# Kernel tuning notes

Measured on AMD Instinct MI355X. Metric: run time of the kernel, lower is better.

The kernel has to match this reference:

```python
import jax, jax.numpy as jnp
import numpy as np
from jax import lax

T, B, F, H = 128, 256, 512, 1024
NEG_SLOPE = 0.01  # torch LeakyReLU default


def leaky_relu(x):
    return jnp.where(x >= 0, x, NEG_SLOPE * x)


def setup_inputs() -> dict:
    key = jax.random.key(0)
    ks = jax.random.split(key, 10)
    s1 = 1.0 / np.sqrt(F)
    sh = 1.0 / np.sqrt(H)
    return {
        "x": jax.random.normal(ks[0], (T, B, F), dtype=jnp.float32),
        "dones": jax.random.randint(ks[1], (T, B), 0, 2, dtype=jnp.int32),
        "W1": jax.random.uniform(ks[2], (H, F), jnp.float32, -s1, s1),
        "b1": jax.random.uniform(ks[3], (H,), jnp.float32, -s1, s1),
        "W_ih": jax.random.uniform(ks[4], (4 * H, H), jnp.float32, -sh, sh),
        "W_hh": jax.random.uniform(ks[5], (4 * H, H), jnp.float32, -sh, sh),
        "b_ih": jax.random.uniform(ks[6], (4 * H,), jnp.float32, -sh, sh),
        "b_hh": jax.random.uniform(ks[7], (4 * H,), jnp.float32, -sh, sh),
        "Wv": jax.random.uniform(ks[8], (1, H), jnp.float32, -sh, sh),
        "bv": jax.random.uniform(ks[9], (1,), jnp.float32, -sh, sh),
    }


def _forward(x, dones, W1, b1, W_ih, W_hh, b_ih, b_hh, Wv, bv):
    # shared_net: Linear + LeakyReLU, applied to all timesteps at once
    shared = leaky_relu(jnp.einsum("tbf,hf->tbh", x, W1) + b1)  # [T,B,H]
    # precompute input contribution to all gates (i,f,g,o order as in torch)
    x_gates = jnp.einsum("tbh,gh->tbg", shared, W_ih) + b_ih + b_hh  # [T,B,4H]
    reset = (dones == 0).astype(x.dtype)[:, :, None]  # [T,B,1], 0 where done

    def step(carry, inp):
        h, c = carry  # [B,H] each
        xg, m = inp
        # mask-reset hidden state where episode ended, then detach (torch .detach())
        h = lax.stop_gradient(h * m)
        c = lax.stop_gradient(c * m)
        gates = xg + h @ W_hh.T  # [B,4H]
        i, f, g, o = jnp.split(gates, 4, axis=-1)
        i = jax.nn.sigmoid(i)
        f = jax.nn.sigmoid(f)
        g = jnp.tanh(g)
        o = jax.nn.sigmoid(o)
        c = f * c + i * g
        h = o * jnp.tanh(c)
        return (h, c), h

    h0 = jnp.zeros((x.shape[1], W_hh.shape[1]), x.dtype)
    (hT, cT), hs = lax.scan(step, (h0, h0), (x_gates, reset))
    value = leaky_relu(hs) @ Wv.T + bv  # [T,B,1]
    hidden = jnp.stack([hT, cT], axis=0)  # [2*num_layers, B, H]
    return value, hidden


def reference(x, dones, W1, b1, W_ih, W_hh, b_ih, b_hh, Wv, bv):
    return _forward(x, dones, W1, b1, W_ih, W_hh, b_ih, b_hh, Wv, bv)
```

## Files before the change

### kernel.cpp

```cpp
#include <hip/hip_runtime.h>
#include <cstdint>
#include <cstddef>

#define T_DIM 128
#define B_DIM 256
#define F_DIM 512
#define H_DIM 1024
#define G_DIM 4096

typedef unsigned short u16;
typedef unsigned short u16x8 __attribute__((ext_vector_type(8)));
typedef unsigned short u16x4 __attribute__((ext_vector_type(4)));
typedef __bf16 bf16x8 __attribute__((ext_vector_type(8)));
typedef float f32x4 __attribute__((ext_vector_type(4)));
typedef unsigned long long u64;

__device__ __forceinline__ float bf2f(u16 u) {
    union { unsigned v; float f; } x; x.v = ((unsigned)u) << 16; return x.f;
}
__device__ __forceinline__ u16 f2bf(float f) {
    union { float f; unsigned v; } x; x.f = f;
    return (u16)((x.v + 0x7fffu + ((x.v >> 16) & 1u)) >> 16);
}

__device__ __forceinline__ f32x4 mfma16(u16x8 a, u16x8 b, f32x4 c) {
    return __builtin_amdgcn_mfma_f32_16x16x32_bf16(
        __builtin_bit_cast(bf16x8, a), __builtin_bit_cast(bf16x8, b), c, 0, 0, 0);
}

template <int AUX>
__device__ __forceinline__ void gl_lds16(const void* g, void* s) {
    __builtin_amdgcn_global_load_lds(
        (const __attribute__((address_space(1))) void*)g,
        (__attribute__((address_space(3))) void*)s, 16, 0, AUX);
}

__device__ __forceinline__ float sigm(float x) { return 1.0f / (1.0f + __expf(-x)); }
__device__ __forceinline__ float tanh_fast(float x) {
    float e = __expf(2.0f * x);
    return 1.0f - 2.0f / (e + 1.0f);
}

template <int EPI>
__global__ __launch_bounds__(256) void gemm_bt128(
    const u16* __restrict__ A, const u16* __restrict__ B,
    const float* __restrict__ bias, u16* __restrict__ C, int K, int N) {
    __shared__ __align__(16) u16 smem[128 * 136];
    u16* lA = smem;
    u16* lB = smem + 8192;
    const int lane = threadIdx.x & 63;
    const int wave = threadIdx.x >> 6;
    const int wr = wave >> 1, wc = wave & 1;
    const int bm = blockIdx.x, bn = blockIdx.y;
    f32x4 acc[4][4] = {};
    const int srow = lane >> 3;
    const int scol = (lane & 7) * 8;
    const u16* Abase = A + (size_t)(bm * 128 + srow) * K + scol;
    const u16* Bbase = B + (size_t)(bn * 128 + srow) * K + scol;

    for (int k0 = 0; k0 < K; k0 += 64) {
#pragma unroll
        for (int j = 0; j < 4; ++j) {
            int chunk = wave * 4 + j;
            gl_lds16<0>(Abase + (size_t)(chunk * 8) * K + k0, lA + chunk * 512);
            gl_lds16<0>(Bbase + (size_t)(chunk * 8) * K + k0, lB + chunk * 512);
        }
        __syncthreads();
        const u16* pA = lA + (wr * 64 + (lane & 15)) * 64 + (lane >> 4) * 8;
        const u16* pB = lB + (wc * 64 + (lane & 15)) * 64 + (lane >> 4) * 8;
#pragma unroll
        for (int kk = 0; kk < 2; ++kk) {
            u16x8 a[4], b[4];
#pragma unroll
            for (int m = 0; m < 4; ++m) a[m] = *(const u16x8*)(pA + m * 1024 + kk * 32);
#pragma unroll
            for (int n = 0; n < 4; ++n) b[n] = *(const u16x8*)(pB + n * 1024 + kk * 32);
#pragma unroll
            for (int m = 0; m < 4; ++m)
#pragma unroll
                for (int n = 0; n < 4; ++n)
                    acc[m][n] = mfma16(a[m], b[n], acc[m][n]);
        }
        __syncthreads();
    }
#pragma unroll
    for (int n = 0; n < 4; ++n) {
        int cc = wc * 64 + n * 16 + (lane & 15);
        float bv = bias[bn * 128 + cc];
#pragma unroll
        for (int m = 0; m < 4; ++m) {
            int rr = wr * 64 + m * 16 + ((lane >> 4) * 4);
#pragma unroll
            for (int i = 0; i < 4; ++i) {
                float v = acc[m][n][i] + bv;
                if (EPI == 1) v = (v >= 0.0f) ? v : 0.01f * v;
                smem[(rr + i) * 136 + cc] = f2bf(v);
            }
        }
    }
    __syncthreads();
#pragma unroll
    for (int p = 0; p < 8; ++p) {
        int rr = p * 16 + wave * 4 + (lane >> 4);
        int cc = (lane & 15) * 8;
        u16x8 v = *(const u16x8*)(smem + rr * 136 + cc);
        *(u16x8*)(C + (size_t)(bm * 128 + rr) * N + bn * 128 + cc) = v;
    }
}


__device__ __forceinline__ void stage_chunk_blk(const char* hinB, int bm, char* buf,
                                                int kc, int wave, int lane) {
#pragma unroll
    for (int j = 0; j < 8; ++j) {
        int hr = wave * 8 + j;
        int r = hr * 2 + (lane >> 5);
        int sc = ((lane & 31) * 16) ^ ((r & 7) << 4);
        int cbg = kc * 512 + sc;
        gl_lds16<17>(hinB + (size_t)(cbg >> 5) * 8192 + bm * 2048 + r * 32 + (cbg & 31),
                     buf + (size_t)hr * 1024);
    }
}

__global__ __launch_bounds__(256, 1) void lstm_seq(
    const u16* __restrict__ xg, const u16* __restrict__ Whh,
    const int* __restrict__ dones, const float* __restrict__ Wv,
    u16* __restrict__ h0, u16* __restrict__ h1,
    float* __restrict__ cbuf, float* __restrict__ hbuf,
    float* __restrict__ value, int* __restrict__ flags,
    float* __restrict__ vpartial, int t0, int nt, int first) {
    __shared__ __align__(16) char sm[65536];
    float* lepi = (float*)sm;
    char* hbB = sm + 17408;
    float* vpB = (float*)(sm + 19456);
    const int tid = threadIdx.x;
    const int lane = tid & 63, wave = tid >> 6;
    const int bm = blockIdx.x & 3, bn = blockIdx.x >> 2;
    const int sw = (lane & 7) << 4;

    u16x8 breg[32];
    {
        const u16* wrow = Whh + (size_t)(bn * 64 + wave * 16 + (lane & 15)) * H_DIM +
                          (lane >> 4) * 8;
#pragma unroll
        for (int s = 0; s < 32; ++s) breg[s] = *(const u16x8*)(wrow + s * 32);
    }

    const int r = tid & 63;
    const int ublk = tid >> 6;
    const int bg = bm * 64 + r;
    const int ucol = bn * 16 + ublk * 4;
    float wv[4], c[4];
#pragma unroll
    for (int uu = 0; uu < 4; ++uu) wv[uu] = Wv[ucol + uu];
    if (first) {
        c[0] = c[1] = c[2] = c[3] = 0.0f;
    } else {
        float4 cv = *(const float4*)(cbuf + (size_t)bg * H_DIM + ucol);
        c[0] = cv.x; c[1] = cv.y; c[2] = cv.z; c[3] = cv.w;
    }

    const int rl = lane & 15;
    const int ko = (lane >> 4) * 16;

    for (int tt = 0; tt < nt; ++tt) {
        const int t = t0 + tt;
        const char* hinB = (const char*)((t & 1) ? h1 : h0);
        u16* houtB = (t & 1) ? h0 : h1;

        auto poll16 = [&](int kc) {
            if (t > 0) {
                const int fi = bm * 64 + kc * 16 + (lane & 15);
                while (__hip_atomic_load(&flags[fi], __ATOMIC_RELAXED,
                                         __HIP_MEMORY_SCOPE_AGENT) < t)
                    __builtin_amdgcn_s_sleep(1);
            }
        };

        const int done = dones[t * B_DIM + bg];
        u16x4 xv[4];
#pragma unroll
        for (int uu = 0; uu < 4; ++uu)
            xv[uu] = *(const u16x4*)(xg + (size_t)tt * B_DIM * G_DIM +
                                     (size_t)bg * G_DIM + bn * 64 + (ublk * 4 + uu) * 4);

        poll16(0);
        stage_chunk_blk(hinB, bm, sm, 0, wave, lane);
        poll16(1);
        __syncthreads();

        f32x4 acc[4] = {};
#pragma unroll
        for (int kc = 0; kc < 4; ++kc) {
            char* buf = sm + (kc & 1) * 32768;
            if (kc < 3) stage_chunk_blk(hinB, bm, sm + ((kc + 1) & 1) * 32768, kc + 1,
                                        wave, lane);
#pragma unroll
            for (int s2 = 0; s2 < 8; ++s2) {
                int kb2 = s2 * 64 + ko;
#pragma unroll
                for (int m = 0; m < 4; ++m) {
                    u16x8 a = *(const u16x8*)(buf + (m * 16 + rl) * 512 + (kb2 ^ sw));
                    acc[m] = mfma16(a, breg[kc * 8 + s2], acc[m]);
                }
            }
            if (kc < 2) poll16(kc + 2);
            if (kc < 3) __syncthreads();
        }

        if (t > 0 && tid < 64) {
            const float* vp = vpartial + (size_t)((t - 1) & 1) * 65536 +
                              (size_t)lane * 1024 + (size_t)(bm * 64 + bn) * 4;
            union { u64 u; float f[2]; } ua, ub;
            ua.u = __hip_atomic_load((const u64*)vp, __ATOMIC_RELAXED,
                                     __HIP_MEMORY_SCOPE_AGENT);
            ub.u = __hip_atomic_load((const u64*)(vp + 2), __ATOMIC_RELAXED,
                                     __HIP_MEMORY_SCOPE_AGENT);
            float s = ua.f[0] + ua.f[1] + ub.f[0] + ub.f[1];
#pragma unroll
            for (int m2 = 32; m2 >= 1; m2 >>= 1) s += __shfl_xor(s, m2);
            if (tid == 0) value[(t - 1) * B_DIM + bm * 64 + bn] += s;
        }

#pragma unroll
        for (int m = 0; m < 4; ++m)
#pragma unroll
            for (int i = 0; i < 4; ++i)
                lepi[(m * 16 + (lane >> 4) * 4 + i) * 65 + wave * 16 + rl] = acc[m][i];

        const float mb = (done == 0) ? 1.0f : 0.0f;
        float vpart = 0.0f;
        u16x4 hb;
        float hf[4];
#pragma unroll
        for (int uu = 0; uu < 4; ++uu) {
            const float* gp = &lepi[r * 65 + (ublk * 4 + uu) * 4];
            float gi = bf2f(xv[uu][0]) + mb * gp[0];
            float gf = bf2f(xv[uu][1]) + mb * gp[1];
            float gg = bf2f(xv[uu][2]) + mb * gp[2];
            float go = bf2f(xv[uu][3]) + mb * gp[3];
            float i_ = sigm(gi), f_ = sigm(gf), g_ = tanh_fast(gg), o_ = sigm(go);
            float cn = f_ * (mb * c[uu]) + i_ * g_;
            float hn = o_ * tanh_fast(cn);
            c[uu] = cn; hf[uu] = hn;
            hb[uu] = f2bf(hn);
            float lr = (hn >= 0.0f) ? hn : 0.01f * hn;
            vpart += lr * wv[uu];
        }
        *(u16x4*)(hbB + r * 32 + ublk * 8) = hb;
        vpB[r * 4 + ublk] = vpart;
        if (t == T_DIM - 1)
            *(float4*)(hbuf + (size_t)bg * H_DIM + ucol) = make_float4(hf[0], hf[1], hf[2], hf[3]);
        __syncthreads();

        {
            u64 hv = *(const u64*)(hbB + tid * 8);
            __hip_atomic_store((u64*)((char*)houtB + (size_t)bn * 8192 + bm * 2048 + tid * 8),
                               hv, __ATOMIC_RELAXED, __HIP_MEMORY_SCOPE_AGENT);
            if (tid < 64) {
                const u64* pv = (const u64*)vpB + tid * 2;
                u64 v0 = pv[0], v1 = pv[1];
                float* dv = vpartial + (size_t)(t & 1) * 65536 + (size_t)bn * 1024 +
                            bm * 256 + tid * 4;
                __hip_atomic_store((u64*)dv, v0, __ATOMIC_RELAXED, __HIP_MEMORY_SCOPE_AGENT);
                __hip_atomic_store((u64*)dv + 1, v1, __ATOMIC_RELAXED, __HIP_MEMORY_SCOPE_AGENT);
            }
        }
        __syncthreads();
        if (tid == 0)
            __hip_atomic_store(&flags[bm * 64 + bn], t + 1, __ATOMIC_RELAXED,
                               __HIP_MEMORY_SCOPE_AGENT);
    }
    *(float4*)(cbuf + (size_t)bg * H_DIM + ucol) = make_float4(c[0], c[1], c[2], c[3]);

    if (t0 + nt == T_DIM && tid < 64) {
        while (__hip_atomic_load(&flags[bm * 64 + lane], __ATOMIC_RELAXED,
                                 __HIP_MEMORY_SCOPE_AGENT) < T_DIM)
            __builtin_amdgcn_s_sleep(1);
        const float* vp = vpartial + (size_t)((T_DIM - 1) & 1) * 65536 +
                          (size_t)lane * 1024 + (size_t)(bm * 64 + bn) * 4;
        union { u64 u; float f[2]; } ua, ub;
        ua.u = __hip_atomic_load((const u64*)vp, __ATOMIC_RELAXED, __HIP_MEMORY_SCOPE_AGENT);
        ub.u = __hip_atomic_load((const u64*)(vp + 2), __ATOMIC_RELAXED,
                                 __HIP_MEMORY_SCOPE_AGENT);
        float s = ua.f[0] + ua.f[1] + ub.f[0] + ub.f[1];
#pragma unroll
        for (int m2 = 32; m2 >= 1; m2 >>= 1) s += __shfl_xor(s, m2);
        if (tid == 0) value[(T_DIM - 1) * B_DIM + bm * 64 + bn] += s;
    }
}

__global__ void k_cast_bf16(const float* __restrict__ in, u16* __restrict__ out, int n4) {
    int i = blockIdx.x * 256 + threadIdx.x;
    if (i < n4) {
        float4 v = *(const float4*)(in + (size_t)i * 4);
        u16x4 o;
        o[0] = f2bf(v.x); o[1] = f2bf(v.y); o[2] = f2bf(v.z); o[3] = f2bf(v.w);
        *(u16x4*)(out + (size_t)i * 4) = o;
    }
}

__global__ void k_permute_w(const float* __restrict__ W, u16* __restrict__ Wp) {
    int row = blockIdx.x;
    int rin = (row & 3) * H_DIM + (row >> 2);
    int c = threadIdx.x * 4;
    float4 v = *(const float4*)(W + (size_t)rin * H_DIM + c);
    u16x4 o;
    o[0] = f2bf(v.x); o[1] = f2bf(v.y); o[2] = f2bf(v.z); o[3] = f2bf(v.w);
    *(u16x4*)(Wp + (size_t)row * H_DIM + c) = o;
}

__global__ void k_prep_bias(const float* __restrict__ b_ih, const float* __restrict__ b_hh,
                            float* __restrict__ bc) {
    int i = blockIdx.x * 256 + threadIdx.x;
    int n = i >> 2, q = i & 3;
    bc[i] = b_ih[q * H_DIM + n] + b_hh[q * H_DIM + n];
}

__global__ void k_init(float* __restrict__ value, const float* __restrict__ bv,
                       u16* __restrict__ h0, int* __restrict__ flags) {
    int i = blockIdx.x * 256 + threadIdx.x;
    if (i < B_DIM * H_DIM) h0[i] = 0;
    if (i < T_DIM * B_DIM) value[i] = *bv;
    if (i < 256) flags[i] = 0;
}

extern "C" void kernel_launch(void* const* d_in, const int* in_sizes, int n_in,
                              void* d_out, int out_size, void* d_ws, size_t ws_size,
                              hipStream_t stream) {
    const float* x     = (const float*)d_in[0];
    const int*   dones = (const int*)d_in[1];
    const float* W1    = (const float*)d_in[2];
    const float* b1    = (const float*)d_in[3];
    const float* W_ih  = (const float*)d_in[4];
    const float* W_hh  = (const float*)d_in[5];
    const float* b_ih  = (const float*)d_in[6];
    const float* b_hh  = (const float*)d_in[7];
    const float* Wv    = (const float*)d_in[8];
    const float* bv    = (const float*)d_in[9];

    float* out   = (float*)d_out;
    float* value = out;
    float* hbuf  = out + (size_t)T_DIM * B_DIM;
    float* cbuf  = hbuf + (size_t)B_DIM * H_DIM;

    const size_t per_nt = (size_t)(F_DIM + H_DIM + G_DIM) * B_DIM * 2;
    const size_t fixed = (size_t)H_DIM * F_DIM * 2 + 2 * (size_t)G_DIM * H_DIM * 2 +
                         G_DIM * 4 + 2 * (size_t)B_DIM * H_DIM * 2 +
                         2 * 65536 * 4 + 8192;
    int nt = 2;
    for (int cand = 64; cand >= 2; cand >>= 1)
        if (fixed + (size_t)cand * per_nt + 65536 <= ws_size) { nt = cand; break; }
    if (nt > T_DIM) nt = T_DIM;

    char* ws = (char*)d_ws;
    size_t off = 0;
    auto alloc = [&](size_t bytes) {
        void* p = ws + off;
        off = (off + bytes + 255) & ~(size_t)255;
        return p;
    };
    u16*   x_bf   = (u16*)alloc((size_t)nt * B_DIM * F_DIM * 2);
    u16*   shr    = (u16*)alloc((size_t)nt * B_DIM * H_DIM * 2);
    u16*   xg     = (u16*)alloc((size_t)nt * B_DIM * G_DIM * 2);
    u16*   W1b    = (u16*)alloc((size_t)H_DIM * F_DIM * 2);
    u16*   Wihp   = (u16*)alloc((size_t)G_DIM * H_DIM * 2);
    u16*   Whhp   = (u16*)alloc((size_t)G_DIM * H_DIM * 2);
    float* bcomb  = (float*)alloc((size_t)G_DIM * 4);
    u16*   hping  = (u16*)alloc((size_t)B_DIM * H_DIM * 2);
    u16*   hpong  = (u16*)alloc((size_t)B_DIM * H_DIM * 2);
    int*   flags  = (int*)alloc(256 * 4);
    float* vpart  = (float*)alloc(2 * 65536 * 4);

    k_cast_bf16<<<(H_DIM * F_DIM / 4) / 256, 256, 0, stream>>>(W1, W1b, H_DIM * F_DIM / 4);
    k_permute_w<<<G_DIM, 256, 0, stream>>>(W_ih, Wihp);
    k_permute_w<<<G_DIM, 256, 0, stream>>>(W_hh, Whhp);
    k_prep_bias<<<G_DIM / 256, 256, 0, stream>>>(b_ih, b_hh, bcomb);
    k_init<<<(B_DIM * H_DIM) / 256, 256, 0, stream>>>(value, bv, hping, flags);

    for (int t0 = 0; t0 < T_DIM; t0 += nt) {
        int m = nt * B_DIM;
        int n4 = m * F_DIM / 4;
        k_cast_bf16<<<n4 / 256, 256, 0, stream>>>(x + (size_t)t0 * B_DIM * F_DIM, x_bf, n4);
        gemm_bt128<1><<<dim3(m / 128, H_DIM / 128), 256, 0, stream>>>(
            x_bf, W1b, b1, shr, F_DIM, H_DIM);
        gemm_bt128<0><<<dim3(m / 128, G_DIM / 128), 256, 0, stream>>>(
            shr, Wihp, bcomb, xg, H_DIM, G_DIM);

        lstm_seq<<<256, 256, 0, stream>>>(
            xg, Whhp, dones, Wv, hping, hpong, cbuf, hbuf, value, flags, vpart,
            t0, nt, (t0 == 0) ? 1 : 0);
    }
}
```

Before: 1.608 ms.

## Overlap next chunk's input GEMMs with the LSTM recurrence in one fused kernel

The sequential LSTM kernel now launches with extra blocks (512 total). Blocks beyond 256 compute the shared-layer and input-gate GEMMs for the next time chunk into a double-buffered xg buffer, while the first 256 blocks run the recurrence for the current chunk. Per-row-tile atomic counters order the two GEMM stages. The input cast is hoisted to a single up-front launch, and the chunk size is fixed at 16 timesteps instead of being derived from workspace size. This hides the per-chunk GEMM and cast launches behind the latency-bound recurrence, but needs 512 co-resident blocks and spin-waits, which may compete with the recurrence blocks for CUs and bandwidth.

```diff
diff --git a/kernel.cpp b/kernel.cpp
--- a/kernel.cpp
+++ b/kernel.cpp
@@ -7,6 +7,7 @@
 #define F_DIM 512
 #define H_DIM 1024
 #define G_DIM 4096
+#define NT    16
 
 typedef unsigned short u16;
 typedef unsigned short u16x8 __attribute__((ext_vector_type(8)));
@@ -41,17 +42,16 @@
     return 1.0f - 2.0f / (e + 1.0f);
 }
 
-template <int EPI>
-__global__ __launch_bounds__(256) void gemm_bt128(
-    const u16* __restrict__ A, const u16* __restrict__ B,
-    const float* __restrict__ bias, u16* __restrict__ C, int K, int N) {
-    __shared__ __align__(16) u16 smem[128 * 136];
+template <int EPI, int WT, int AUXA>
+__device__ void gemm_tile(char* smraw, const u16* __restrict__ A,
+                          const u16* __restrict__ B, const float* __restrict__ bias,
+                          u16* __restrict__ C, int K, int N, int bm, int bn) {
+    u16* smem = (u16*)smraw;
     u16* lA = smem;
     u16* lB = smem + 8192;
     const int lane = threadIdx.x & 63;
     const int wave = threadIdx.x >> 6;
     const int wr = wave >> 1, wc = wave & 1;
-    const int bm = blockIdx.x, bn = blockIdx.y;
     f32x4 acc[4][4] = {};
     const int srow = lane >> 3;
     const int scol = (lane & 7) * 8;
@@ -62,7 +62,7 @@
 #pragma unroll
         for (int j = 0; j < 4; ++j) {
             int chunk = wave * 4 + j;
-            gl_lds16<0>(Abase + (size_t)(chunk * 8) * K + k0, lA + chunk * 512);
+            gl_lds16<AUXA>(Abase + (size_t)(chunk * 8) * K + k0, lA + chunk * 512);
             gl_lds16<0>(Bbase + (size_t)(chunk * 8) * K + k0, lB + chunk * 512);
         }
         __syncthreads();
@@ -104,38 +104,66 @@
         int rr = p * 16 + wave * 4 + (lane >> 4);
         int cc = (lane & 15) * 8;
         u16x8 v = *(const u16x8*)(smem + rr * 136 + cc);
-        *(u16x8*)(C + (size_t)(bm * 128 + rr) * N + bn * 128 + cc) = v;
-    }
-}
-
-
-__device__ __forceinline__ void stage_chunk_blk(const char* hinB, int bm, char* buf,
-                                                int kc, int wave, int lane) {
-#pragma unroll
-    for (int j = 0; j < 8; ++j) {
-        int hr = wave * 8 + j;
-        int r = hr * 2 + (lane >> 5);
-        int sc = ((lane & 31) * 16) ^ ((r & 7) << 4);
-        int cbg = kc * 512 + sc;
-        gl_lds16<17>(hinB + (size_t)(cbg >> 5) * 8192 + bm * 2048 + r * 32 + (cbg & 31),
-                     buf + (size_t)hr * 1024);
-    }
-}
-
-__global__ __launch_bounds__(256, 1) void lstm_seq(
+        u16* dst = C + (size_t)(bm * 128 + rr) * N + bn * 128 + cc;
+        if (WT) {
+            union { u16x8 h; u64 q[2]; } u; u.h = v;
+            __hip_atomic_store((u64*)dst, u.q[0], __ATOMIC_RELAXED, __HIP_MEMORY_SCOPE_AGENT);
+            __hip_atomic_store((u64*)dst + 1, u.q[1], __ATOMIC_RELAXED, __HIP_MEMORY_SCOPE_AGENT);
+        } else {
+            *(u16x8*)dst = v;
+        }
+    }
+    __syncthreads();
+}
+
+template <int EPI>
+__global__ __launch_bounds__(256) void gemm_bt128(
+    const u16* __restrict__ A, const u16* __restrict__ B,
+    const float* __restrict__ bias, u16* __restrict__ C, int K, int N) {
+    __shared__ __align__(16) char smem[128 * 136 * 2];
+    gemm_tile<EPI, 0, 0>(smem, A, B, bias, C, K, N, blockIdx.x, blockIdx.y);
+}
+
+__global__ __launch_bounds__(256, 1) void fused_step(
     const u16* __restrict__ xg, const u16* __restrict__ Whh,
     const int* __restrict__ dones, const float* __restrict__ Wv,
     u16* __restrict__ h0, u16* __restrict__ h1,
     float* __restrict__ cbuf, float* __restrict__ hbuf,
     float* __restrict__ value, int* __restrict__ flags,
-    float* __restrict__ vpartial, int t0, int nt, int first) {
+    float* __restrict__ vpartial, int t0, int nt, int first,
+    int MT, int kidx, const u16* __restrict__ x_bf, const u16* __restrict__ W1b,
+    const float* __restrict__ b1, u16* __restrict__ shr,
+    const u16* __restrict__ Wih, const float* __restrict__ bcomb,
+    u16* __restrict__ xg_next, int* __restrict__ g1cnt) {
     __shared__ __align__(16) char sm[65536];
+    const int bid = blockIdx.x;
+    const int tid = threadIdx.x;
+
+    if (bid >= 256) {
+        if (MT == 0) return;
+        const int g = bid - 256;
+        for (int id = g; id < MT * 8; id += 256) {
+            gemm_tile<1, 1, 0>(sm, x_bf, W1b, b1, shr, F_DIM, H_DIM, id >> 3, id & 7);
+            if (tid == 0)
+                __hip_atomic_fetch_add(&g1cnt[id >> 3], 1, __ATOMIC_RELAXED,
+                                       __HIP_MEMORY_SCOPE_AGENT);
+        }
+        const int target = 8 * (kidx + 1);
+        for (int id = g; id < MT * 32; id += 256) {
+            int bmp = id >> 5, bnp = id & 31;
+            while (__hip_atomic_load(&g1cnt[bmp], __ATOMIC_RELAXED,
+                                     __HIP_MEMORY_SCOPE_AGENT) < target)
+                __builtin_amdgcn_s_sleep(2);
+            gemm_tile<0, 0, 17>(sm, shr, Wih, bcomb, xg_next, H_DIM, G_DIM, bmp, bnp);
+        }
+        return;
+    }
+
     float* lepi = (float*)sm;
     char* hbB = sm + 17408;
     float* vpB = (float*)(sm + 19456);
-    const int tid = threadIdx.x;
     const int lane = tid & 63, wave = tid >> 6;
-    const int bm = blockIdx.x & 3, bn = blockIdx.x >> 2;
+    const int bm = bid & 3, bn = bid >> 2;
     const int sw = (lane & 7) << 4;
 
     u16x8 breg[32];
@@ -176,6 +204,17 @@
                     __builtin_amdgcn_s_sleep(1);
             }
         };
+        auto stage_chunk_blk = [&](char* buf, int kc) {
+#pragma unroll
+            for (int j = 0; j < 8; ++j) {
+                int hr = wave * 8 + j;
+                int rr = hr * 2 + (lane >> 5);
+                int sc = ((lane & 31) * 16) ^ ((rr & 7) << 4);
+                int cbg = kc * 512 + sc;
+                gl_lds16<17>(hinB + (size_t)(cbg >> 5) * 8192 + bm * 2048 + rr * 32 +
+                             (cbg & 31), buf + (size_t)hr * 1024);
+            }
+        };
 
         const int done = dones[t * B_DIM + bg];
         u16x4 xv[4];
@@ -185,7 +224,7 @@
                                      (size_t)bg * G_DIM + bn * 64 + (ublk * 4 + uu) * 4);
 
         poll16(0);
-        stage_chunk_blk(hinB, bm, sm, 0, wave, lane);
+        stage_chunk_blk(sm, 0);
         poll16(1);
         __syncthreads();
 
@@ -193,8 +232,7 @@
 #pragma unroll
         for (int kc = 0; kc < 4; ++kc) {
             char* buf = sm + (kc & 1) * 32768;
-            if (kc < 3) stage_chunk_blk(hinB, bm, sm + ((kc + 1) & 1) * 32768, kc + 1,
-                                        wave, lane);
+            if (kc < 3) stage_chunk_blk(sm + ((kc + 1) & 1) * 32768, kc + 1);
 #pragma unroll
             for (int s2 = 0; s2 < 8; ++s2) {
                 int kb2 = s2 * 64 + ko;
@@ -318,11 +356,13 @@
 }
 
 __global__ void k_init(float* __restrict__ value, const float* __restrict__ bv,
-                       u16* __restrict__ h0, int* __restrict__ flags) {
+                       u16* __restrict__ h0, int* __restrict__ flags,
+                       int* __restrict__ g1cnt) {
     int i = blockIdx.x * 256 + threadIdx.x;
     if (i < B_DIM * H_DIM) h0[i] = 0;
     if (i < T_DIM * B_DIM) value[i] = *bv;
     if (i < 256) flags[i] = 0;
+    if (i < 128) g1cnt[i] = 0;
 }
 
 extern "C" void kernel_launch(void* const* d_in, const int* in_sizes, int n_in,
@@ -344,15 +384,6 @@
     float* hbuf  = out + (size_t)T_DIM * B_DIM;
     float* cbuf  = hbuf + (size_t)B_DIM * H_DIM;
 
-    const size_t per_nt = (size_t)(F_DIM + H_DIM + G_DIM) * B_DIM * 2;
-    const size_t fixed = (size_t)H_DIM * F_DIM * 2 + 2 * (size_t)G_DIM * H_DIM * 2 +
-                         G_DIM * 4 + 2 * (size_t)B_DIM * H_DIM * 2 +
-                         2 * 65536 * 4 + 8192;
-    int nt = 2;
-    for (int cand = 64; cand >= 2; cand >>= 1)
-        if (fixed + (size_t)cand * per_nt + 65536 <= ws_size) { nt = cand; break; }
-    if (nt > T_DIM) nt = T_DIM;
-
     char* ws = (char*)d_ws;
     size_t off = 0;
     auto alloc = [&](size_t bytes) {
@@ -360,9 +391,14 @@
         off = (off + bytes + 255) & ~(size_t)255;
         return p;
     };
-    u16*   x_bf   = (u16*)alloc((size_t)nt * B_DIM * F_DIM * 2);
+    const int nt = NT;
+    const int chunks = T_DIM / nt;
+    const int MT = 2 * nt;
+
+    u16*   x_bf   = (u16*)alloc((size_t)T_DIM * B_DIM * F_DIM * 2);
     u16*   shr    = (u16*)alloc((size_t)nt * B_DIM * H_DIM * 2);
-    u16*   xg     = (u16*)alloc((size_t)nt * B_DIM * G_DIM * 2);
+    u16*   xgA    = (u16*)alloc((size_t)nt * B_DIM * G_DIM * 2);
+    u16*   xgB    = (u16*)alloc((size_t)nt * B_DIM * G_DIM * 2);
     u16*   W1b    = (u16*)alloc((size_t)H_DIM * F_DIM * 2);
     u16*   Wihp   = (u16*)alloc((size_t)G_DIM * H_DIM * 2);
     u16*   Whhp   = (u16*)alloc((size_t)G_DIM * H_DIM * 2);
@@ -370,25 +406,30 @@
     u16*   hping  = (u16*)alloc((size_t)B_DIM * H_DIM * 2);
     u16*   hpong  = (u16*)alloc((size_t)B_DIM * H_DIM * 2);
     int*   flags  = (int*)alloc(256 * 4);
+    int*   g1cnt  = (int*)alloc(128 * 4);
     float* vpart  = (float*)alloc(2 * 65536 * 4);
 
+    k_cast_bf16<<<(T_DIM * B_DIM * F_DIM / 4) / 256, 256, 0, stream>>>(
+        x, x_bf, T_DIM * B_DIM * F_DIM / 4);
     k_cast_bf16<<<(H_DIM * F_DIM / 4) / 256, 256, 0, stream>>>(W1, W1b, H_DIM * F_DIM / 4);
     k_permute_w<<<G_DIM, 256, 0, stream>>>(W_ih, Wihp);
     k_permute_w<<<G_DIM, 256, 0, stream>>>(W_hh, Whhp);
     k_prep_bias<<<G_DIM / 256, 256, 0, stream>>>(b_ih, b_hh, bcomb);
-    k_init<<<(B_DIM * H_DIM) / 256, 256, 0, stream>>>(value, bv, hping, flags);
-
-    for (int t0 = 0; t0 < T_DIM; t0 += nt) {
-        int m = nt * B_DIM;
-        int n4 = m * F_DIM / 4;
-        k_cast_bf16<<<n4 / 256, 256, 0, stream>>>(x + (size_t)t0 * B_DIM * F_DIM, x_bf, n4);
-        gemm_bt128<1><<<dim3(m / 128, H_DIM / 128), 256, 0, stream>>>(
-            x_bf, W1b, b1, shr, F_DIM, H_DIM);
-        gemm_bt128<0><<<dim3(m / 128, G_DIM / 128), 256, 0, stream>>>(
-            shr, Wihp, bcomb, xg, H_DIM, G_DIM);
-
-        lstm_seq<<<256, 256, 0, stream>>>(
-            xg, Whhp, dones, Wv, hping, hpong, cbuf, hbuf, value, flags, vpart,
-            t0, nt, (t0 == 0) ? 1 : 0);
-    }
-}
+    k_init<<<(B_DIM * H_DIM) / 256, 256, 0, stream>>>(value, bv, hping, flags, g1cnt);
+
+    gemm_bt128<1><<<dim3(MT, H_DIM / 128), 256, 0, stream>>>(
+        x_bf, W1b, b1, shr, F_DIM, H_DIM);
+    gemm_bt128<0><<<dim3(MT, G_DIM / 128), 256, 0, stream>>>(
+        shr, Wihp, bcomb, xgA, H_DIM, G_DIM);
+
+    for (int k = 0; k < chunks; ++k) {
+        const u16* xg_cur = (k & 1) ? xgB : xgA;
+        u16* xg_nxt = (k & 1) ? xgA : xgB;
+        int mt = (k + 1 < chunks) ? MT : 0;
+        fused_step<<<512, 256, 0, stream>>>(
+            xg_cur, Whhp, dones, Wv, hping, hpong, cbuf, hbuf, value, flags, vpart,
+            k * nt, nt, (k == 0) ? 1 : 0,
+            mt, k, x_bf + (size_t)(k + 1) * nt * B_DIM * F_DIM, W1b, b1, shr,
+            Wihp, bcomb, xg_nxt, g1cnt);
+    }
+}
```

New measurement: 1.912 ms. 1.19x slower.
